# Kernel tuning notes

Measured on AMD Instinct MI355X. Metric: run time of the kernel, lower is better.

The kernel has to match this reference:

```python
import math
import jax, jax.numpy as jnp
import numpy as np

N = 8192
D = 512
TOPK = 20


def setup_inputs() -> dict:
    key = jax.random.key(0)
    k1, k2, k3, k4 = jax.random.split(key, 4)
    h = jax.random.normal(k1, (N, D), dtype=jnp.float32)
    prior_adj = jax.random.normal(k2, (N, N), dtype=jnp.float32)
    # Linear(d, d, bias=False) weights, PyTorch convention: y = x @ W.T
    scale = 1.0 / math.sqrt(D)
    W_q = jax.random.normal(k3, (D, D), dtype=jnp.float32) * scale
    W_k = jax.random.normal(k4, (D, D), dtype=jnp.float32) * scale
    prior_scale = jnp.asarray(0.1, dtype=jnp.float32)
    return {"h": h, "prior_adj": prior_adj, "W_q": W_q, "W_k": W_k,
            "prior_scale": prior_scale}


def reference(h, prior_adj, W_q, W_k, prior_scale):
    # Q = h @ W_q.T, K = h @ W_k.T  (nn.Linear convention)
    Q = h @ W_q.T                                      # [N, D]
    K = h @ W_k.T                                      # [N, D]
    logits = (Q @ K.T) / math.sqrt(D)                  # [N, N]
    logits = logits + prior_scale * prior_adj
    n = logits.shape[0]
    neg_inf = jnp.float32(-jnp.inf)
    # mask diagonal (no self-edges)
    eye = jnp.eye(n, dtype=bool)
    logits = jnp.where(eye, neg_inf, logits)
    k = min(TOPK, n - 1)
    # per-row top-k indices, scatter into a boolean keep-mask
    _, idx = jax.lax.top_k(logits, k)                  # [N, k]
    mask = jnp.zeros((n, n), dtype=bool)
    mask = mask.at[jnp.arange(n)[:, None], idx].set(True)
    masked_logits = jnp.where(mask, logits, neg_inf)
    attn = jax.nn.softmax(masked_logits, axis=-1)      # rows have >=1 finite entry
    attn = jnp.nan_to_num(attn, nan=0.0)
    return attn
```

## Files before the change

kernel.cpp:

```cpp
#include <hip/hip_runtime.h>
#include <hip/hip_bf16.h>
#include <math.h>


#define MARGIN 0.20f
#define RSQRT_D 0.04419417382415922f

typedef __attribute__((ext_vector_type(8))) short short8;
typedef __attribute__((ext_vector_type(4))) float f32x4;

__device__ __forceinline__ unsigned long long ordkey(float v, int j) {
  unsigned u = __float_as_uint(v);
  u = (u & 0x80000000u) ? ~u : (u | 0x80000000u);
  return ((unsigned long long)u << 32) | (unsigned)(8191 - j);
}

__global__ __launch_bounds__(256) void k1_qk(const float* __restrict__ h,
                                             const float* __restrict__ Wq,
                                             const float* __restrict__ Wk,
                                             float* __restrict__ Q32,
                                             float* __restrict__ K32,
                                             __hip_bfloat16* __restrict__ Qb,
                                             __hip_bfloat16* __restrict__ Kb) {
  __shared__ float hs[64][17];
  __shared__ float wqs[64][17];
  __shared__ float wks[64][17];
  const int t = threadIdx.x;
  const int tx = t & 15, ty = t >> 4;
  const int i0 = blockIdx.y * 64, e0 = blockIdx.x * 64;
  const int r = t >> 2, c4 = (t & 3) * 4;
  float aq[4][4] = {};
  float ak[4][4] = {};
  for (int k0 = 0; k0 < 512; k0 += 16) {
    __syncthreads();
    {
      const float4 hv = *(const float4*)&h[(size_t)(i0 + r) * 512 + k0 + c4];
      hs[r][c4 + 0] = hv.x; hs[r][c4 + 1] = hv.y; hs[r][c4 + 2] = hv.z; hs[r][c4 + 3] = hv.w;
      const float4 qv = *(const float4*)&Wq[(size_t)(e0 + r) * 512 + k0 + c4];
      wqs[r][c4 + 0] = qv.x; wqs[r][c4 + 1] = qv.y; wqs[r][c4 + 2] = qv.z; wqs[r][c4 + 3] = qv.w;
      const float4 kv = *(const float4*)&Wk[(size_t)(e0 + r) * 512 + k0 + c4];
      wks[r][c4 + 0] = kv.x; wks[r][c4 + 1] = kv.y; wks[r][c4 + 2] = kv.z; wks[r][c4 + 3] = kv.w;
    }
    __syncthreads();
#pragma unroll
    for (int dd = 0; dd < 16; dd++) {
      float hv[4], qv[4], kv[4];
#pragma unroll
      for (int a = 0; a < 4; a++) hv[a] = hs[ty * 4 + a][dd];
#pragma unroll
      for (int b = 0; b < 4; b++) { qv[b] = wqs[tx * 4 + b][dd]; kv[b] = wks[tx * 4 + b][dd]; }
#pragma unroll
      for (int a = 0; a < 4; a++)
#pragma unroll
        for (int b = 0; b < 4; b++) {
          aq[a][b] = fmaf(hv[a], qv[b], aq[a][b]);
          ak[a][b] = fmaf(hv[a], kv[b], ak[a][b]);
        }
    }
  }
#pragma unroll
  for (int a = 0; a < 4; a++)
#pragma unroll
    for (int b = 0; b < 4; b++) {
      const size_t gi = (size_t)(i0 + ty * 4 + a) * 512 + e0 + tx * 4 + b;
      Q32[gi] = aq[a][b];
      K32[gi] = ak[a][b];
      Qb[gi] = __float2bfloat16(aq[a][b]);
      Kb[gi] = __float2bfloat16(ak[a][b]);
    }
}

__global__ __launch_bounds__(256) void k2_logits(const short* __restrict__ Qb,
                                                 const short* __restrict__ Kb,
                                                 const float* __restrict__ prior,
                                                 const float* __restrict__ psp,
                                                 float* __restrict__ out) {
  __shared__ short As[128 * 32];
  __shared__ short Bs[128 * 32];
  const int t = threadIdx.x;
  const int w = t >> 6, l = t & 63;
  const int wr = w >> 1, wc = w & 1;
  const int i0 = blockIdx.y * 128, j0 = blockIdx.x * 128;

  f32x4 acc[4][4];
#pragma unroll
  for (int a = 0; a < 4; a++)
#pragma unroll
    for (int b = 0; b < 4; b++) acc[a][b] = (f32x4){0.f, 0.f, 0.f, 0.f};

  const int rA = t >> 2;
  const int cA = (t & 3) * 8;
  const short* gA = Qb + (size_t)(i0 + rA) * 512 + cA;
  const short* gB = Kb + (size_t)(j0 + rA) * 512 + cA;
  char* lA = (char*)As + w * 1024;
  char* lB = (char*)Bs + w * 1024;

  for (int k0 = 0; k0 < 512; k0 += 32) {
    __syncthreads();
    __builtin_amdgcn_global_load_lds((__attribute__((address_space(1))) void*)(gA + k0),
                                     (__attribute__((address_space(3))) void*)(lA), 16, 0, 0);
    __builtin_amdgcn_global_load_lds((__attribute__((address_space(1))) void*)(gA + 64 * 512 + k0),
                                     (__attribute__((address_space(3))) void*)(lA + 4096), 16, 0, 0);
    __builtin_amdgcn_global_load_lds((__attribute__((address_space(1))) void*)(gB + k0),
                                     (__attribute__((address_space(3))) void*)(lB), 16, 0, 0);
    __builtin_amdgcn_global_load_lds((__attribute__((address_space(1))) void*)(gB + 64 * 512 + k0),
                                     (__attribute__((address_space(3))) void*)(lB + 4096), 16, 0, 0);
    __syncthreads();

    const int m = l & 15, kq = (l >> 4) * 8;
    short8 af[4], bfr[4];
#pragma unroll
    for (int f = 0; f < 4; f++) {
      af[f]  = *(const short8*)&As[(wr * 64 + f * 16 + m) * 32 + kq];
      bfr[f] = *(const short8*)&Bs[(wc * 64 + f * 16 + m) * 32 + kq];
    }
#pragma unroll
    for (int fr = 0; fr < 4; fr++)
#pragma unroll
      for (int fc = 0; fc < 4; fc++)
        acc[fr][fc] = __builtin_amdgcn_mfma_f32_16x16x32_bf16(af[fr], bfr[fc], acc[fr][fc], 0, 0, 0);
  }

  const float psv = psp[0];
  const int m = l & 15, q = l >> 4;
#pragma unroll
  for (int fr = 0; fr < 4; fr++) {
    const int grb = i0 + wr * 64 + fr * 16 + q * 4;
#pragma unroll
    for (int fc = 0; fc < 4; fc++) {
      const int gc = j0 + wc * 64 + fc * 16 + m;
#pragma unroll
      for (int r = 0; r < 4; r++) {
        const int gr = grb + r;
        const size_t off = (size_t)gr * 8192 + gc;
        float v = acc[fr][fc][r] * RSQRT_D + psv * prior[off];
        if (gr == gc) v = -__builtin_inff();
        out[off] = v;
      }
    }
  }
}

__device__ __forceinline__ float blockmax_f(float v, float* sred, int t) {
#pragma unroll
  for (int off = 32; off > 0; off >>= 1) v = fmaxf(v, __shfl_down(v, off));
  __syncthreads();
  if ((t & 63) == 0) sred[t >> 6] = v;
  __syncthreads();
  return fmaxf(fmaxf(sred[0], sred[1]), fmaxf(sred[2], sred[3]));
}
__device__ __forceinline__ int blocksum_i(int v, int* sred, int t) {
#pragma unroll
  for (int off = 32; off > 0; off >>= 1) v += __shfl_down(v, off);
  __syncthreads();
  if ((t & 63) == 0) sred[t >> 6] = v;
  __syncthreads();
  return sred[0] + sred[1] + sred[2] + sred[3];
}

__global__ __launch_bounds__(256) void k3_topk(float* out,
                                               const float* __restrict__ Q32,
                                               const float* __restrict__ K32,
                                               const float* __restrict__ prior,
                                               const float* __restrict__ psp) {
  const int row = blockIdx.x;
  const int t = threadIdx.x;
  __shared__ __align__(16) float qrow[512];
  __shared__ float fred[4];
  __shared__ int ired[4];
  __shared__ int candi[256];
  __shared__ unsigned long long keys[256];
  __shared__ int ncand_s;
  __shared__ float sel20v[20];
  __shared__ int sel20i[20];
  __shared__ double ex[20];
  __shared__ float wout[20];

  const float psv = psp[0];
  float* lrow = out + (size_t)row * 8192;

  float r[32];
  {
    const float4* lr4 = (const float4*)lrow;
#pragma unroll
    for (int u = 0; u < 8; u++) {
      const float4 v = lr4[t + 256 * u];
      r[u * 4 + 0] = v.x; r[u * 4 + 1] = v.y; r[u * 4 + 2] = v.z; r[u * 4 + 3] = v.w;
    }
  }
  for (int e = t; e < 512; e += 256) qrow[e] = Q32[(size_t)row * 512 + e];
  if (t == 0) ncand_s = 0;

  float pm = r[0];
#pragma unroll
  for (int u = 1; u < 32; u++) pm = fmaxf(pm, r[u]);
  const float M = blockmax_f(pm, fred, t);

  float lo = M - 8.0f, hi = M;
  {
    int c = 0;
#pragma unroll
    for (int u = 0; u < 32; u++) c += (r[u] >= lo) ? 1 : 0;
    int ctot = blocksum_i(c, ired, t);
    float w = 8.0f;
    int guard = 0;
    while (ctot < 20 && guard < 140) {
      w *= 2.0f; lo = M - w;
      c = 0;
#pragma unroll
      for (int u = 0; u < 32; u++) c += (r[u] >= lo) ? 1 : 0;
      ctot = blocksum_i(c, ired, t);
      guard++;
    }
  }
  float T = lo;
  for (int it = 0; it < 15; it++) {
    const float mid = 0.5f * (lo + hi);
    int c = 0;
#pragma unroll
    for (int u = 0; u < 32; u++) c += (r[u] >= mid) ? 1 : 0;
    const int ctot = blocksum_i(c, ired, t);
    if (ctot >= 20) {
      lo = mid; T = mid;
      if (ctot <= 48) break;
    } else {
      hi = mid;
    }
  }

  const float Tc = T - MARGIN;
#pragma unroll
  for (int u2 = 0; u2 < 32; u2++) {
    if (r[u2] >= Tc) {
      const int p = atomicAdd(&ncand_s, 1);
      if (p < 256) candi[p] = 4 * t + 1024 * (u2 >> 2) + (u2 & 3);
    }
  }
  __syncthreads();
  const int ncand = min(ncand_s, 256);

  float Lf = -__builtin_inff();
  int myi = 0x7fffffff;
  unsigned long long mykey = 0ull;
  if (t < ncand) {
    myi = candi[t];
    const float* kr = &K32[(size_t)myi * 512];
    float s = 0.f;
#pragma unroll 8
    for (int k = 0; k < 512; k += 4) {
      const float4 kv = *(const float4*)&kr[k];
      s = fmaf(qrow[k + 0], kv.x, s);
      s = fmaf(qrow[k + 1], kv.y, s);
      s = fmaf(qrow[k + 2], kv.z, s);
      s = fmaf(qrow[k + 3], kv.w, s);
    }
    Lf = __fdiv_rn(s, 22.62741699796952f);
    Lf = __fadd_rn(Lf, __fmul_rn(psv, prior[(size_t)row * 8192 + myi]));
    mykey = ordkey(Lf, myi);
  }
  keys[t] = mykey;
  __syncthreads();

  if (t < ncand) {
    int rank = 0;
    for (int jj = 0; jj < ncand; jj++) rank += (keys[jj] > mykey) ? 1 : 0;
    if (rank < 20) { sel20v[rank] = Lf; sel20i[rank] = myi; }
  }
  __syncthreads();

  if (t < 20) {
    float m2 = sel20v[0];
    for (int k = 1; k < 20; k++) m2 = fmaxf(m2, sel20v[k]);
    ex[t] = exp((double)sel20v[t] - (double)m2);
  }
  __syncthreads();
  if (t == 0) {
    double Z = 0.0;
    for (int k = 0; k < 20; k++) Z += ex[k];
    for (int k = 0; k < 20; k++) wout[k] = (float)(ex[k] / Z);
  }
  __syncthreads();

  const float4 z = {0.f, 0.f, 0.f, 0.f};
  for (int c = t; c < 2048; c += 256) ((float4*)lrow)[c] = z;
  __syncthreads();
  if (t < 20) lrow[sel20i[t]] = wout[t];
}

extern "C" void kernel_launch(void* const* d_in, const int* in_sizes, int n_in,
                              void* d_out, int out_size, void* d_ws, size_t ws_size,
                              hipStream_t stream) {
  const float* h     = (const float*)d_in[0];
  const float* prior = (const float*)d_in[1];
  const float* Wq    = (const float*)d_in[2];
  const float* Wk    = (const float*)d_in[3];
  const float* ps    = (const float*)d_in[4];
  float* out = (float*)d_out;

  char* ws = (char*)d_ws;
  float* Q32 = (float*)ws;
  float* K32 = (float*)(ws + ((size_t)16 << 20));
  __hip_bfloat16* Qb = (__hip_bfloat16*)(ws + ((size_t)32 << 20));
  __hip_bfloat16* Kb = (__hip_bfloat16*)(ws + ((size_t)40 << 20));

  k1_qk<<<dim3(8, 128), 256, 0, stream>>>(h, Wq, Wk, Q32, K32, Qb, Kb);
  k2_logits<<<dim3(64, 64), 256, 0, stream>>>((const short*)Qb, (const short*)Kb,
                                              prior, ps, out);
  k3_topk<<<8192, 256, 0, stream>>>(out, Q32, K32, prior, ps);
}
```

Before: 889.6 us.

## Store bf16 logits, retile QK projection, swizzle logits grid, zero rows early

The logits kernel now writes bf16 values into the first half of each output row instead of fp32. The top-k kernel reads that half, zeroes the whole row in registers-first order, and rebuilds fp32 candidates from bf16, which cuts logits write and read traffic roughly in half. The QK projection kernel moves to 128-row tiles with float4 LDS loads and a strided thread mapping, and the logits grid gets an XCD-style block swizzle. Candidate filtering already uses a margin and exact fp32 rescoring, but coarser bf16 pre-filter values could drop true top-k entries if the margin is too small.

```diff
diff --git a/kernel.cpp b/kernel.cpp
--- a/kernel.cpp
+++ b/kernel.cpp
@@ -7,6 +7,7 @@
 #define RSQRT_D 0.04419417382415922f
 
 typedef __attribute__((ext_vector_type(8))) short short8;
+typedef __attribute__((ext_vector_type(8))) unsigned short ushort8;
 typedef __attribute__((ext_vector_type(4))) float f32x4;
 
 __device__ __forceinline__ unsigned long long ordkey(float v, int j) {
@@ -22,47 +23,48 @@
                                              float* __restrict__ K32,
                                              __hip_bfloat16* __restrict__ Qb,
                                              __hip_bfloat16* __restrict__ Kb) {
-  __shared__ float hs[64][17];
-  __shared__ float wqs[64][17];
-  __shared__ float wks[64][17];
+  __shared__ float hs[128][20];
+  __shared__ float wqs[64][20];
+  __shared__ float wks[64][20];
   const int t = threadIdx.x;
   const int tx = t & 15, ty = t >> 4;
-  const int i0 = blockIdx.y * 64, e0 = blockIdx.x * 64;
+  const int i0 = blockIdx.y * 128, e0 = blockIdx.x * 64;
   const int r = t >> 2, c4 = (t & 3) * 4;
-  float aq[4][4] = {};
-  float ak[4][4] = {};
+  float aq[8][4] = {};
+  float ak[8][4] = {};
   for (int k0 = 0; k0 < 512; k0 += 16) {
     __syncthreads();
-    {
-      const float4 hv = *(const float4*)&h[(size_t)(i0 + r) * 512 + k0 + c4];
-      hs[r][c4 + 0] = hv.x; hs[r][c4 + 1] = hv.y; hs[r][c4 + 2] = hv.z; hs[r][c4 + 3] = hv.w;
-      const float4 qv = *(const float4*)&Wq[(size_t)(e0 + r) * 512 + k0 + c4];
-      wqs[r][c4 + 0] = qv.x; wqs[r][c4 + 1] = qv.y; wqs[r][c4 + 2] = qv.z; wqs[r][c4 + 3] = qv.w;
-      const float4 kv = *(const float4*)&Wk[(size_t)(e0 + r) * 512 + k0 + c4];
-      wks[r][c4 + 0] = kv.x; wks[r][c4 + 1] = kv.y; wks[r][c4 + 2] = kv.z; wks[r][c4 + 3] = kv.w;
-    }
+    *(float4*)&hs[r][c4]      = *(const float4*)&h[(size_t)(i0 + r) * 512 + k0 + c4];
+    *(float4*)&hs[64 + r][c4] = *(const float4*)&h[(size_t)(i0 + 64 + r) * 512 + k0 + c4];
+    *(float4*)&wqs[r][c4]     = *(const float4*)&Wq[(size_t)(e0 + r) * 512 + k0 + c4];
+    *(float4*)&wks[r][c4]     = *(const float4*)&Wk[(size_t)(e0 + r) * 512 + k0 + c4];
     __syncthreads();
 #pragma unroll
-    for (int dd = 0; dd < 16; dd++) {
-      float hv[4], qv[4], kv[4];
-#pragma unroll
-      for (int a = 0; a < 4; a++) hv[a] = hs[ty * 4 + a][dd];
-#pragma unroll
-      for (int b = 0; b < 4; b++) { qv[b] = wqs[tx * 4 + b][dd]; kv[b] = wks[tx * 4 + b][dd]; }
-#pragma unroll
-      for (int a = 0; a < 4; a++)
-#pragma unroll
-        for (int b = 0; b < 4; b++) {
-          aq[a][b] = fmaf(hv[a], qv[b], aq[a][b]);
-          ak[a][b] = fmaf(hv[a], kv[b], ak[a][b]);
-        }
-    }
-  }
-#pragma unroll
-  for (int a = 0; a < 4; a++)
+    for (int d0 = 0; d0 < 16; d0 += 4) {
+      f32x4 hv[8], qv[4], kv[4];
+#pragma unroll
+      for (int a = 0; a < 8; a++) hv[a] = *(const f32x4*)&hs[ty + 16 * a][d0];
+#pragma unroll
+      for (int b = 0; b < 4; b++) {
+        qv[b] = *(const f32x4*)&wqs[tx + 16 * b][d0];
+        kv[b] = *(const f32x4*)&wks[tx + 16 * b][d0];
+      }
+#pragma unroll
+      for (int kk = 0; kk < 4; kk++)
+#pragma unroll
+        for (int a = 0; a < 8; a++)
+#pragma unroll
+          for (int b = 0; b < 4; b++) {
+            aq[a][b] = fmaf(hv[a][kk], qv[b][kk], aq[a][b]);
+            ak[a][b] = fmaf(hv[a][kk], kv[b][kk], ak[a][b]);
+          }
+    }
+  }
+#pragma unroll
+  for (int a = 0; a < 8; a++)
 #pragma unroll
     for (int b = 0; b < 4; b++) {
-      const size_t gi = (size_t)(i0 + ty * 4 + a) * 512 + e0 + tx * 4 + b;
+      const size_t gi = (size_t)(i0 + ty + 16 * a) * 512 + e0 + tx + 16 * b;
       Q32[gi] = aq[a][b];
       K32[gi] = ak[a][b];
       Qb[gi] = __float2bfloat16(aq[a][b]);
@@ -80,7 +82,9 @@
   const int t = threadIdx.x;
   const int w = t >> 6, l = t & 63;
   const int wr = w >> 1, wc = w & 1;
-  const int i0 = blockIdx.y * 128, j0 = blockIdx.x * 128;
+  int flat = blockIdx.y * 64 + blockIdx.x;
+  flat = (flat & 7) * 512 + (flat >> 3);
+  const int i0 = (flat >> 6) * 128, j0 = (flat & 63) * 128;
 
   f32x4 acc[4][4];
 #pragma unroll
@@ -130,12 +134,12 @@
     for (int fc = 0; fc < 4; fc++) {
       const int gc = j0 + wc * 64 + fc * 16 + m;
 #pragma unroll
-      for (int r = 0; r < 4; r++) {
-        const int gr = grb + r;
+      for (int rr = 0; rr < 4; rr++) {
+        const int gr = grb + rr;
         const size_t off = (size_t)gr * 8192 + gc;
-        float v = acc[fr][fc][r] * RSQRT_D + psv * prior[off];
+        float v = acc[fr][fc][rr] * RSQRT_D + psv * prior[off];
         if (gr == gc) v = -__builtin_inff();
-        out[off] = v;
+        ((__hip_bfloat16*)(out + (size_t)gr * 8192))[gc] = __float2bfloat16(v);
       }
     }
   }
@@ -179,14 +183,24 @@
   const float psv = psp[0];
   float* lrow = out + (size_t)row * 8192;
 
-  float r[32];
+  float4 fv[4];
   {
     const float4* lr4 = (const float4*)lrow;
 #pragma unroll
-    for (int u = 0; u < 8; u++) {
-      const float4 v = lr4[t + 256 * u];
-      r[u * 4 + 0] = v.x; r[u * 4 + 1] = v.y; r[u * 4 + 2] = v.z; r[u * 4 + 3] = v.w;
-    }
+    for (int u = 0; u < 4; u++) fv[u] = lr4[t + 256 * u];
+  }
+  {
+    const float4 z = {0.f, 0.f, 0.f, 0.f};
+#pragma unroll
+    for (int u = 0; u < 8; u++) ((float4*)lrow)[t + 256 * u] = z;
+  }
+  float r[32];
+#pragma unroll
+  for (int u = 0; u < 4; u++) {
+    const ushort8 us = *(const ushort8*)&fv[u];
+#pragma unroll
+    for (int e = 0; e < 8; e++)
+      r[u * 8 + e] = __uint_as_float(((unsigned)us[e]) << 16);
   }
   for (int e = t; e < 512; e += 256) qrow[e] = Q32[(size_t)row * 512 + e];
   if (t == 0) ncand_s = 0;
@@ -233,7 +247,7 @@
   for (int u2 = 0; u2 < 32; u2++) {
     if (r[u2] >= Tc) {
       const int p = atomicAdd(&ncand_s, 1);
-      if (p < 256) candi[p] = 4 * t + 1024 * (u2 >> 2) + (u2 & 3);
+      if (p < 256) candi[p] = 8 * t + 2048 * (u2 >> 3) + (u2 & 7);
     }
   }
   __syncthreads();
@@ -280,10 +294,6 @@
     for (int k = 0; k < 20; k++) wout[k] = (float)(ex[k] / Z);
   }
   __syncthreads();
-
-  const float4 z = {0.f, 0.f, 0.f, 0.f};
-  for (int c = t; c < 2048; c += 256) ((float4*)lrow)[c] = z;
-  __syncthreads();
   if (t < 20) lrow[sel20i[t]] = wout[t];
 }
 
@@ -303,7 +313,7 @@
   __hip_bfloat16* Qb = (__hip_bfloat16*)(ws + ((size_t)32 << 20));
   __hip_bfloat16* Kb = (__hip_bfloat16*)(ws + ((size_t)40 << 20));
 
-  k1_qk<<<dim3(8, 128), 256, 0, stream>>>(h, Wq, Wk, Q32, K32, Qb, Kb);
+  k1_qk<<<dim3(8, 64), 256, 0, stream>>>(h, Wq, Wk, Q32, K32, Qb, Kb);
   k2_logits<<<dim3(64, 64), 256, 0, stream>>>((const short*)Qb, (const short*)Kb,
                                               prior, ps, out);
   k3_topk<<<8192, 256, 0, stream>>>(out, Q32, K32, prior, ps);
```

After: 811.7 us. -8.8%, faster.
